# Kernel tuning notes

Hardware: AMD Instinct MI355X
Metric: run time of the kernel (lower is better)

Reference implementation:

```python
import jax, jax.numpy as jnp
import numpy as np

B, T, D = 4, 8160, 1024
N, H = 8, 128            # heads, units_per_head (D == N*H)
W = 12                   # block_size
LEFT_CTX = 13            # atten_left_context
L = LEFT_CTX - 1         # left context frames beyond current position
R = 0                    # atten_right_context
C = W + L + R            # context_size = 24
CAP = 50.0               # attention_logits_soft_capping


def _timing_signal(pos, channels):
    # sinusoidal embedding, channels even (1024)
    pos = pos.astype(jnp.float32)
    nt = channels // 2
    inc = np.log(10000.0) / max(nt - 1, 1)
    inv = jnp.exp(jnp.arange(nt, dtype=jnp.float32) * -inc)
    st = pos[:, :, None] * inv[None, None, :]
    return jnp.concatenate([jnp.sin(st), jnp.cos(st)], axis=2)


def _extract_block_context(x, block_size, left, right, pad_val):
    # x: [B, T, ...] -> [B, num_blocks, context_size, ...]
    pads = [(0, 0)] * x.ndim
    pads[1] = (left, right + block_size - 1)
    xp = jnp.pad(x, pads, constant_values=jnp.asarray(pad_val, x.dtype))
    frame_len = block_size + left + right
    num_frames = (xp.shape[1] - frame_len) // block_size + 1
    idx = jnp.arange(num_frames)[:, None] * block_size + jnp.arange(frame_len)[None, :]
    return jnp.take(xp, idx, axis=1)


def _convert_to_block(x, block_size):
    b, t = x.shape[0], x.shape[1]
    nb = t // block_size  # T chosen as multiple of block_size
    return x.reshape((b, nb, block_size) + x.shape[2:])


def setup_inputs() -> dict:
    key = jax.random.key(0)
    ks = jax.random.split(key, 6)
    x = jax.random.normal(ks[0], (B, T, D), dtype=jnp.float32)
    mask = jnp.ones((B, T), dtype=bool)
    i = jnp.arange(W)[:, None]
    j = jnp.arange(C)[None, :]
    causal_valid_mask = (j >= i) & (j - i <= L + R)  # [W, C]
    s = 1.0 / np.sqrt(D)
    wq = jax.random.normal(ks[1], (D, D), dtype=jnp.float32) * s
    wk = jax.random.normal(ks[2], (D, D), dtype=jnp.float32) * s
    wv = jax.random.normal(ks[3], (D, D), dtype=jnp.float32) * s
    pos_proj = jax.random.normal(ks[4], (D, N, H), dtype=jnp.float32) * s
    return {"x": x, "mask": mask, "causal_valid_mask": causal_valid_mask,
            "wq": wq, "wk": wk, "wv": wv, "pos_proj": pos_proj}


def reference(x, mask, causal_valid_mask, wq, wk, wv, pos_proj):
    b, t, d = x.shape
    u = t // W
    q = jnp.einsum('btd,df->btf', x, wq).reshape(b, t, N, H)
    k = jnp.einsum('btd,df->btf', x, wk).reshape(b, t, N, H)
    v = jnp.einsum('btd,df->btf', x, wv).reshape(b, t, N, H)

    q_blk = _convert_to_block(q, W) * (H ** -0.5)        # [B,U,W,N,H]
    k_ctx = _extract_block_context(k, W, L, R, 0.0)      # [B,U,C,N,H]
    v_ctx = _extract_block_context(v, W, L, R, 0.0)      # [B,U,C,N,H]

    # term A+C: content logits
    term_ac = jnp.einsum('BuwNH,BucNH->BNuwc', q_blk, k_ctx)

    # term B+D: relative position logits via skew trick
    pos = jnp.arange(L, -R - 1, -1)[None, :]             # [1, L+R+1]
    sin_emb = _timing_signal(pos, D)                     # [1, L+R+1, D]
    sin_emb = jnp.einsum('fd,dnh->fnh', sin_emb[0], pos_proj)  # [F,N,H]
    term_bd = jnp.einsum('BuwNH,FNH->BNuwF', q_blk, sin_emb)   # [B,N,U,W,F]
    term_bd = jnp.pad(term_bd, ((0, 0),) * 4 + ((0, C + 1 - (L + R + 1)),))
    term_bd = term_bd.reshape(b, N, u, W * (C + 1))[:, :, :, :W * C]
    term_bd = term_bd.reshape(b, N, u, W, C)

    logits = term_ac + term_bd
    logits = CAP * jnp.tanh(logits / CAP)

    mask_ctx = _extract_block_context(mask, W, L, R, False)    # [B,U,C]
    valid = mask_ctx[:, None, :, None, :] & causal_valid_mask[None, None, None, :, :]
    logits = jnp.where(valid, logits, jnp.asarray(-1e9, logits.dtype))
    probs = jax.nn.softmax(logits, axis=-1)              # [B,N,U,W,C]

    out = jnp.einsum('BNuwc,BucNH->BuwNH', probs, v_ctx)
    return out.reshape(b, u * W, N, H)[:, :t]            # [B,T,N,H]
```

## Files before the change

### kernel.cpp

```cpp
#include <hip/hip_runtime.h>
#include <cstdint>
#include <cstddef>


typedef __bf16 bf16_t;
typedef float  floatx4 __attribute__((ext_vector_type(4)));
typedef __bf16 bf16x8  __attribute__((ext_vector_type(8)));
typedef __bf16 bf16x4  __attribute__((ext_vector_type(4)));
typedef _Float16 f16x8 __attribute__((ext_vector_type(8)));

#define GLDS16(gp, lp)                                                        \
  __builtin_amdgcn_global_load_lds(                                           \
      (const __attribute__((address_space(1))) void*)(gp),                    \
      (__attribute__((address_space(3))) void*)(lp), 16, 0, 0)

static constexpr int kT     = 8160;
static constexpr int kM     = 4 * kT;
static constexpr int kU     = kT / 12;
static constexpr int kNC    = 3200;

__global__ __launch_bounds__(256) void convert_x(const float* __restrict__ X,
                                                 bf16_t* __restrict__ Xb) {
  const size_t i = ((size_t)blockIdx.x * 256 + threadIdx.x) * 8;
  float4 a = *(const float4*)(X + i);
  float4 b = *(const float4*)(X + i + 4);
  bf16x8 o;
  o[0] = (bf16_t)a.x; o[1] = (bf16_t)a.y; o[2] = (bf16_t)a.z; o[3] = (bf16_t)a.w;
  o[4] = (bf16_t)b.x; o[5] = (bf16_t)b.y; o[6] = (bf16_t)b.z; o[7] = (bf16_t)b.w;
  *(bf16x8*)(Xb + i) = o;
}

__global__ __launch_bounds__(512) void posemb_k(const float* __restrict__ pp,
                                                float* __restrict__ pe) {
  __shared__ float st[1024];
  __shared__ float red[4][128];
  const int d   = blockIdx.x;
  const int fc  = blockIdx.y;
  const int tid = threadIdx.x;
  const float dpos = (float)d;
  for (int i = tid; i < 1024; i += 512) {
    int idx = i & 511;
    float freq = expf(-(float)idx * (9.2103403719761836f / 511.0f));
    float a = dpos * freq;
    st[i] = (i < 512) ? sinf(a) : cosf(a);
  }
  __syncthreads();
  const int part = tid >> 7;
  const int fl   = tid & 127;
  const int f    = fc * 128 + fl;
  float acc = 0.f;
  const int dd0 = part * 256;
  for (int dd = dd0; dd < dd0 + 256; ++dd)
    acc += st[dd] * pp[(size_t)dd * 1024 + f];
  red[part][fl] = acc;
  __syncthreads();
  if (tid < 128)
    pe[(size_t)d * 1024 + f] = red[0][fl] + red[1][fl] + red[2][fl] + red[3][fl];
}

__global__ __launch_bounds__(256) void transpose_w(const float* __restrict__ Wq,
                                                   const float* __restrict__ Wk,
                                                   const float* __restrict__ Wv,
                                                   bf16_t* __restrict__ Wt) {
  __shared__ float tile[64][65];
  const int g = blockIdx.z;
  const float* W = (g == 0) ? Wq : (g == 1) ? Wk : Wv;
  bf16_t* O = Wt + (size_t)g * 1024 * 1024;
  const int k0 = blockIdx.x * 64, n0 = blockIdx.y * 64;
  const int col = threadIdx.x & 63, r4 = threadIdx.x >> 6;
#pragma unroll
  for (int i = 0; i < 16; ++i) {
    int row = i * 4 + r4;
    tile[row][col] = W[(size_t)(k0 + row) * 1024 + n0 + col];
  }
  __syncthreads();
#pragma unroll
  for (int i = 0; i < 16; ++i) {
    int row = i * 4 + r4;
    O[(size_t)(n0 + row) * 1024 + k0 + col] = (bf16_t)tile[col][row];
  }
}

__global__ __launch_bounds__(256) void pe2w(const float* __restrict__ pe,
                                            bf16_t* __restrict__ Wt) {
  const int idx = blockIdx.x;
  const int tid = threadIdx.x;
  bf16_t* out = Wt + (size_t)(3072 + idx) * 1024;
  if (idx >= 104) {
    bf16x4 z = {};
    *(bf16x4*)(out + tid * 4) = z;
    return;
  }
  const int n = idx / 13, d = idx - n * 13;
  __shared__ float peh[128];
  if (tid < 128) peh[tid] = pe[(size_t)d * 1024 + n * 128 + tid];
  __syncthreads();
  float acc[4] = {};
  const bf16_t* wb = Wt + (size_t)(n * 128) * 1024 + tid * 4;
  for (int h = 0; h < 128; ++h) {
    bf16x4 w4 = *(const bf16x4*)(wb + (size_t)h * 1024);
    float s = peh[h];
    acc[0] += s * (float)w4[0];
    acc[1] += s * (float)w4[1];
    acc[2] += s * (float)w4[2];
    acc[3] += s * (float)w4[3];
  }
  bf16x4 o;
  o[0] = (bf16_t)acc[0]; o[1] = (bf16_t)acc[1];
  o[2] = (bf16_t)acc[2]; o[3] = (bf16_t)acc[3];
  *(bf16x4*)(out + tid * 4) = o;
}

__global__ __launch_bounds__(512, 2) void qkv_gemm(const bf16_t* __restrict__ X,
                                                   const bf16_t* __restrict__ Wt,
                                                   bf16_t* __restrict__ QKV) {
  __shared__ __align__(16) bf16_t lds[8][8192];

  const int flat = blockIdx.x;
  const int work = (flat & 7) * 208 + (flat >> 3);
  const int mt = work / 13, nt = work % 13;
  const int m0 = mt * 256, n0 = nt * 256;

  const int tid  = threadIdx.x;
  const int wave = tid >> 6;
  const int lane = tid & 63;
  const int wm   = wave >> 2;
  const int wn   = wave & 3;
  const int qd   = lane >> 4;
  const int lr   = lane & 15;

  const int rr  = tid >> 3;
  const int cg8 = ((tid & 7) ^ (rr & 7)) * 8;
  const bf16_t* aP[4];
  const bf16_t* bP[4];
  {
    int r2 = m0 + 128 + rr, r3 = m0 + 192 + rr;
    aP[0] = X + (size_t)(m0 + rr) * 1024 + cg8;
    aP[1] = X + (size_t)(m0 + 64 + rr) * 1024 + cg8;
    aP[2] = X + (size_t)(r2 < kM ? r2 : 0) * 1024 + cg8;
    aP[3] = X + (size_t)(r3 < kM ? r3 : 0) * 1024 + cg8;
    int s2 = n0 + 128 + rr, s3 = n0 + 192 + rr;
    bP[0] = Wt + (size_t)(n0 + rr) * 1024 + cg8;
    bP[1] = Wt + (size_t)(n0 + 64 + rr) * 1024 + cg8;
    bP[2] = Wt + (size_t)(s2 < kNC ? s2 : 0) * 1024 + cg8;
    bP[3] = Wt + (size_t)(s3 < kNC ? s3 : 0) * 1024 + cg8;
  }

#define STAGE_A(h, t)                                                          \
  do {                                                                         \
    bf16_t* d_ = &lds[((t) & 1) * 4 + (h)][wave * 512];                        \
    GLDS16(aP[2 * (h)]     + (size_t)(t) * 64, d_);                            \
    GLDS16(aP[2 * (h) + 1] + (size_t)(t) * 64, d_ + 4096);                     \
  } while (0)
#define STAGE_B(h, t)                                                          \
  do {                                                                         \
    bf16_t* d_ = &lds[((t) & 1) * 4 + 2 + (h)][wave * 512];                    \
    GLDS16(bP[2 * (h)]     + (size_t)(t) * 64, d_);                            \
    GLDS16(bP[2 * (h) + 1] + (size_t)(t) * 64, d_ + 4096);                     \
  } while (0)

  auto frag = [&](int slot, int r, int cb) -> bf16x8 {
    uint32_t off = (uint32_t)(r * 128 + cb) ^ (uint32_t)((r & 7) << 4);
    return *(const bf16x8*)((const char*)&lds[slot][0] + off);
  };

  floatx4 acc[8][4] = {};

  STAGE_A(0, 0); STAGE_A(1, 0); STAGE_B(0, 0); STAGE_B(1, 0);
  STAGE_B(0, 1); STAGE_B(1, 1);
  asm volatile("s_waitcnt vmcnt(4)" ::: "memory");
  __builtin_amdgcn_s_barrier();

  const int aslot0 = wm;
  const int bslot0 = 2 + (wn >> 1);
  const int brow0  = (wn & 1) * 64;

#pragma unroll 2
  for (int t = 0; t < 16; ++t) {
    const int par = (t & 1) * 4;
    bf16x8 bfrag[4][2];
#pragma unroll
    for (int p = 0; p < 4; ++p) {
      if (p == 0) {
#pragma unroll
        for (int in = 0; in < 4; ++in)
#pragma unroll
          for (int k2 = 0; k2 < 2; ++k2)
            bfrag[in][k2] =
                frag(par + bslot0, brow0 + in * 16 + lr, k2 * 64 + qd * 16);
      }
      bf16x8 afrag[2][2];
#pragma unroll
      for (int i = 0; i < 2; ++i)
#pragma unroll
        for (int k2 = 0; k2 < 2; ++k2)
          afrag[i][k2] =
              frag(par + aslot0, (2 * p + i) * 16 + lr, k2 * 64 + qd * 16);

      if (p == 0)      { if (t < 15) STAGE_A(0, t + 1); }
      else if (p == 1) { if (t < 15) STAGE_A(1, t + 1); }
      else if (p == 2) { if (t < 14) STAGE_B(0, t + 2); }
      else             { if (t < 14) STAGE_B(1, t + 2); }

      if (p == 3) {
        if (t < 14) asm volatile("s_waitcnt vmcnt(4)" ::: "memory");
        else        asm volatile("s_waitcnt vmcnt(0)" ::: "memory");
      }
      __builtin_amdgcn_s_barrier();
      asm volatile("s_waitcnt lgkmcnt(0)" ::: "memory");
      __builtin_amdgcn_sched_barrier(0);

      __builtin_amdgcn_s_setprio(1);
#pragma unroll
      for (int i = 0; i < 2; ++i)
#pragma unroll
        for (int in = 0; in < 4; ++in)
#pragma unroll
          for (int k2 = 0; k2 < 2; ++k2)
            acc[2 * p + i][in] = __builtin_amdgcn_mfma_f32_16x16x32_bf16(
                afrag[i][k2], bfrag[in][k2], acc[2 * p + i][in], 0, 0, 0);
      __builtin_amdgcn_s_setprio(0);
      __builtin_amdgcn_sched_barrier(0);
      __builtin_amdgcn_s_barrier();
    }
  }
#undef STAGE_A
#undef STAGE_B

  const int mBase = m0 + wm * 128 + qd * 4;
  const int nBase = n0 + wn * 64 + lr;
  if (m0 + 256 <= kM && n0 + 256 <= kNC) {
#pragma unroll
    for (int im = 0; im < 8; ++im)
#pragma unroll
      for (int in = 0; in < 4; ++in)
#pragma unroll
        for (int r = 0; r < 4; ++r)
          QKV[(size_t)(mBase + im * 16 + r) * kNC + nBase + in * 16] =
              (bf16_t)acc[im][in][r];
  } else {
#pragma unroll
    for (int im = 0; im < 8; ++im)
#pragma unroll
      for (int in = 0; in < 4; ++in)
#pragma unroll
        for (int r = 0; r < 4; ++r) {
          int m = mBase + im * 16 + r;
          int n = nBase + in * 16;
          if (m < kM && n < kNC)
            QKV[(size_t)m * kNC + n] = (bf16_t)acc[im][in][r];
        }
  }
}

__global__ __launch_bounds__(256) void attn_k(const bf16_t* __restrict__ QKV,
                                              float* __restrict__ OUT) {
  __shared__ __align__(16) bf16_t  Ks[80 * 128];
  __shared__ __align__(16) _Float16 Vt[128 * 128];
  __shared__ __align__(16) unsigned char QP[64 * 256];
  __shared__ float qpes[64 * 16];

  bf16_t*   Qs = (bf16_t*)QP;
  _Float16* Ps = (_Float16*)QP;

  const int flat  = blockIdx.x;
  const int work  = (flat & 7) * 544 + (flat >> 3);
  const int strip = work >> 5;
  const int rest  = work & 31;
  const int n     = rest >> 2;
  const int b     = rest & 3;
  const int u0    = strip * 5;
  const int t0    = u0 * 12 - 12;
  const size_t bbase = (size_t)b * kT;
  const int tid  = threadIdx.x;
  const int mi   = tid >> 6;
  const int lane = tid & 63;
  const int qd   = lane >> 4;
  const int lr   = lane & 15;

  for (int i = tid; i < 64 * 16; i += 256) {
    int row = i >> 4, ch = i & 15;
    bf16x8 q8 = {};
    if (row < 60)
      q8 = *(const bf16x8*)(QKV + (bbase + (u0 * 12 + row)) * kNC + n * 128 + ch * 8);
    int idx = (row * 128 + ch * 8) ^ ((row & 7) << 3);
    *(bf16x8*)(Qs + idx) = q8;
  }
  for (int i = tid; i < 80 * 16; i += 256) {
    int row = i >> 4, ch = i & 15;
    int t = t0 + row;
    bf16x8 k8 = {};
    if (t >= 0 && t < kT)
      k8 = *(const bf16x8*)(QKV + (bbase + t) * kNC + 1024 + n * 128 + ch * 8);
    int idx = (row * 128 + ch * 8) ^ ((row & 7) << 3);
    *(bf16x8*)(Ks + idx) = k8;
  }
  for (int i = tid; i < 96 * 16; i += 256) {
    int c = i >> 4, ch = i & 15;
    int t = t0 + c;
    bf16x8 v8 = {};
    if (c < 80 && t >= 0 && t < kT)
      v8 = *(const bf16x8*)(QKV + (bbase + t) * kNC + 2048 + n * 128 + ch * 8);
#pragma unroll
    for (int jx = 0; jx < 8; ++jx) {
      int h = ch * 8 + jx;
      int idx = (h * 128 + c) ^ ((h & 7) << 3);
      Vt[idx] = (_Float16)(float)v8[jx];
    }
  }
  for (int i = tid; i < 780; i += 256) {
    int m = i / 13, d = i - m * 13;
    qpes[m * 16 + d] =
        (float)QKV[(bbase + (u0 * 12 + m)) * kNC + 3072 + n * 13 + d];
  }
  __syncthreads();

  floatx4 sAcc[2] = {};
  {
    bf16x8 aQ[4];
    const int qrow = mi * 16 + lr;
#pragma unroll
    for (int kk = 0; kk < 4; ++kk) {
      int idx = (qrow * 128 + kk * 32 + qd * 8) ^ ((qrow & 7) << 3);
      aQ[kk] = *(const bf16x8*)(Qs + idx);
    }
#pragma unroll
    for (int ci = 0; ci < 2; ++ci) {
      int krow = (mi + ci) * 16 + lr;
#pragma unroll
      for (int kk = 0; kk < 4; ++kk) {
        int idx = (krow * 128 + kk * 32 + qd * 8) ^ ((krow & 7) << 3);
        bf16x8 bK = *(const bf16x8*)(Ks + idx);
        sAcc[ci] = __builtin_amdgcn_mfma_f32_16x16x32_bf16(aQ[kk], bK, sAcc[ci], 0, 0, 0);
      }
    }
  }

  float pval[2][4];
#pragma unroll
  for (int r = 0; r < 4; ++r) {
    const int m = mi * 16 + qd * 4 + r;
    float sv[2]; bool val[2];
    float mx = -1e30f;
#pragma unroll
    for (int ci = 0; ci < 2; ++ci) {
      int c = (mi + ci) * 16 + lr;
      int d = m + 12 - c;
      int t = t0 + c;
      bool v = (d >= 0) && (d <= 12) && (t >= 0) && (m < 60);
      int qidx = m * 16 + (v ? d : 0);
      float s = (sAcc[ci][r] + qpes[qidx]) * 0.0017677669529663689f;
      s = 50.0f * tanhf(s);
      sv[ci] = v ? s : -1e30f;
      val[ci] = v;
      mx = fmaxf(mx, sv[ci]);
    }
    mx = fmaxf(mx, __shfl_xor(mx, 1));
    mx = fmaxf(mx, __shfl_xor(mx, 2));
    mx = fmaxf(mx, __shfl_xor(mx, 4));
    mx = fmaxf(mx, __shfl_xor(mx, 8));
    float e0 = val[0] ? __expf(sv[0] - mx) : 0.f;
    float e1 = val[1] ? __expf(sv[1] - mx) : 0.f;
    float sm = e0 + e1;
    sm += __shfl_xor(sm, 1);
    sm += __shfl_xor(sm, 2);
    sm += __shfl_xor(sm, 4);
    sm += __shfl_xor(sm, 8);
    float inv = (sm > 0.f) ? 1.0f / sm : 0.f;
    pval[0][r] = e0 * inv;
    pval[1][r] = e1 * inv;
  }

  __syncthreads();
  {
    float4 z = {};
    float4* p4 = (float4*)QP;
    for (int i = tid; i < 1024; i += 256) p4[i] = z;
  }
  __syncthreads();
#pragma unroll
  for (int r = 0; r < 4; ++r) {
    const int m = mi * 16 + qd * 4 + r;
#pragma unroll
    for (int ci = 0; ci < 2; ++ci) {
      int c = (mi + ci) * 16 + lr;
      int idx = (m * 128 + c) ^ ((m & 7) << 3);
      Ps[idx] = (_Float16)pval[ci][r];
    }
  }
  __syncthreads();

  floatx4 oAcc[8] = {};
  const int klo = mi >> 1;
  const int khi = (16 * mi + 27) >> 5;
  const int prow = mi * 16 + lr;
  for (int kk = klo; kk <= khi; ++kk) {
    int pidx = (prow * 128 + kk * 32 + qd * 8) ^ ((prow & 7) << 3);
    f16x8 aP = *(const f16x8*)(Ps + pidx);
#pragma unroll
    for (int hf = 0; hf < 8; ++hf) {
      int vrow = hf * 16 + lr;
      int vidx = (vrow * 128 + kk * 32 + qd * 8) ^ ((vrow & 7) << 3);
      f16x8 bV = *(const f16x8*)(Vt + vidx);
      oAcc[hf] = __builtin_amdgcn_mfma_f32_16x16x32_f16(aP, bV, oAcc[hf], 0, 0, 0);
    }
  }

#pragma unroll
  for (int r = 0; r < 4; ++r) {
    const int m = mi * 16 + qd * 4 + r;
    if (m < 60) {
      float* op = OUT + (bbase + (u0 * 12 + m)) * 1024 + n * 128 + lr;
#pragma unroll
      for (int hf = 0; hf < 8; ++hf)
        op[hf * 16] = oAcc[hf][r];
    }
  }
}

extern "C" void kernel_launch(void* const* d_in, const int* in_sizes, int n_in,
                              void* d_out, int out_size, void* d_ws, size_t ws_size,
                              hipStream_t stream) {
  const float* x  = (const float*)d_in[0];
  const float* wq = (const float*)d_in[3];
  const float* wk = (const float*)d_in[4];
  const float* wv = (const float*)d_in[5];
  const float* pp = (const float*)d_in[6];

  char* ws = (char*)d_ws;
  float*  pe  = (float*)ws;
  bf16_t* Wt  = (bf16_t*)(ws + (1u << 16));
  bf16_t* Xb  = (bf16_t*)(ws + (1u << 16) + 8u * 1024 * 1024);
  bf16_t* QKV = (bf16_t*)(ws + (1u << 16) + 8u * 1024 * 1024 +
                          (size_t)kM * 1024 * 2);
  float* out = (float*)d_out;

  convert_x<<<kM * 1024 / (256 * 8), 256, 0, stream>>>(x, Xb);
  posemb_k<<<dim3(13, 8), 512, 0, stream>>>(pp, pe);
  transpose_w<<<dim3(16, 16, 3), 256, 0, stream>>>(wq, wk, wv, Wt);
  pe2w<<<128, 256, 0, stream>>>(pe, Wt);
  qkv_gemm<<<1664, 512, 0, stream>>>(Xb, Wt, QKV);
  attn_k<<<4352, 256, 0, stream>>>(QKV, out);
}
```

Baseline: 650.8 us.

## Split attention into QK-softmax and banded PV kernels with compact probabilities

Splits the fused attention kernel into two kernels. The first computes QK logits and softmax and writes only the 13 valid banded probabilities per query to a global buffer that reuses the bf16 X workspace. The second computes the PV product as a 13-tap banded sum in fp32 on the vector ALUs. This removes the large transposed-V LDS staging and the mostly-zero PV MFMA. Q loads now go straight to registers, and tanh is computed with exp and no max subtraction. The cost is an extra launch, a global round trip for the probabilities, and softmax with no max shift (safe only because the logits are capped at 50).

After: 588.5 us. -9.6%, faster.

```diff
diff --git a/kernel.cpp b/kernel.cpp
--- a/kernel.cpp
+++ b/kernel.cpp
@@ -7,7 +7,6 @@
 typedef float  floatx4 __attribute__((ext_vector_type(4)));
 typedef __bf16 bf16x8  __attribute__((ext_vector_type(8)));
 typedef __bf16 bf16x4  __attribute__((ext_vector_type(4)));
-typedef _Float16 f16x8 __attribute__((ext_vector_type(8)));
 
 #define GLDS16(gp, lp)                                                        \
   __builtin_amdgcn_global_load_lds(                                           \
@@ -253,15 +252,10 @@
   }
 }
 
-__global__ __launch_bounds__(256) void attn_k(const bf16_t* __restrict__ QKV,
-                                              float* __restrict__ OUT) {
-  __shared__ __align__(16) bf16_t  Ks[80 * 128];
-  __shared__ __align__(16) _Float16 Vt[128 * 128];
-  __shared__ __align__(16) unsigned char QP[64 * 256];
+__global__ __launch_bounds__(256) void qk_soft(const bf16_t* __restrict__ QKV,
+                                               float* __restrict__ Pg) {
+  __shared__ __align__(16) bf16_t Ks[80 * 128];
   __shared__ float qpes[64 * 16];
-
-  bf16_t*   Qs = (bf16_t*)QP;
-  _Float16* Ps = (_Float16*)QP;
 
   const int flat  = blockIdx.x;
   const int work  = (flat & 7) * 544 + (flat >> 3);
@@ -272,41 +266,31 @@
   const int u0    = strip * 5;
   const int t0    = u0 * 12 - 12;
   const size_t bbase = (size_t)b * kT;
+  const int bn    = b * 8 + n;
   const int tid  = threadIdx.x;
   const int mi   = tid >> 6;
   const int lane = tid & 63;
   const int qd   = lane >> 4;
   const int lr   = lane & 15;
 
-  for (int i = tid; i < 64 * 16; i += 256) {
-    int row = i >> 4, ch = i & 15;
-    bf16x8 q8 = {};
-    if (row < 60)
-      q8 = *(const bf16x8*)(QKV + (bbase + (u0 * 12 + row)) * kNC + n * 128 + ch * 8);
-    int idx = (row * 128 + ch * 8) ^ ((row & 7) << 3);
-    *(bf16x8*)(Qs + idx) = q8;
-  }
+  bf16x8 aQ[4];
+  {
+    int tq = u0 * 12 + mi * 16 + lr;
+    if (tq > kT - 1) tq = kT - 1;
+    const bf16_t* qg = QKV + (bbase + tq) * kNC + n * 128;
+#pragma unroll
+    for (int kk = 0; kk < 4; ++kk)
+      aQ[kk] = *(const bf16x8*)(qg + kk * 32 + qd * 8);
+  }
+
   for (int i = tid; i < 80 * 16; i += 256) {
     int row = i >> 4, ch = i & 15;
-    int t = t0 + row;
+    int kt = t0 + row;
     bf16x8 k8 = {};
-    if (t >= 0 && t < kT)
-      k8 = *(const bf16x8*)(QKV + (bbase + t) * kNC + 1024 + n * 128 + ch * 8);
+    if (kt >= 0 && kt < kT)
+      k8 = *(const bf16x8*)(QKV + (bbase + kt) * kNC + 1024 + n * 128 + ch * 8);
     int idx = (row * 128 + ch * 8) ^ ((row & 7) << 3);
     *(bf16x8*)(Ks + idx) = k8;
-  }
-  for (int i = tid; i < 96 * 16; i += 256) {
-    int c = i >> 4, ch = i & 15;
-    int t = t0 + c;
-    bf16x8 v8 = {};
-    if (c < 80 && t >= 0 && t < kT)
-      v8 = *(const bf16x8*)(QKV + (bbase + t) * kNC + 2048 + n * 128 + ch * 8);
-#pragma unroll
-    for (int jx = 0; jx < 8; ++jx) {
-      int h = ch * 8 + jx;
-      int idx = (h * 128 + c) ^ ((h & 7) << 3);
-      Vt[idx] = (_Float16)(float)v8[jx];
-    }
   }
   for (int i = tid; i < 780; i += 256) {
     int m = i / 13, d = i - m * 13;
@@ -316,105 +300,96 @@
   __syncthreads();
 
   floatx4 sAcc[2] = {};
-  {
-    bf16x8 aQ[4];
-    const int qrow = mi * 16 + lr;
+#pragma unroll
+  for (int ci = 0; ci < 2; ++ci) {
+    int krow = (mi + ci) * 16 + lr;
 #pragma unroll
     for (int kk = 0; kk < 4; ++kk) {
-      int idx = (qrow * 128 + kk * 32 + qd * 8) ^ ((qrow & 7) << 3);
-      aQ[kk] = *(const bf16x8*)(Qs + idx);
-    }
-#pragma unroll
-    for (int ci = 0; ci < 2; ++ci) {
-      int krow = (mi + ci) * 16 + lr;
-#pragma unroll
-      for (int kk = 0; kk < 4; ++kk) {
-        int idx = (krow * 128 + kk * 32 + qd * 8) ^ ((krow & 7) << 3);
-        bf16x8 bK = *(const bf16x8*)(Ks + idx);
-        sAcc[ci] = __builtin_amdgcn_mfma_f32_16x16x32_bf16(aQ[kk], bK, sAcc[ci], 0, 0, 0);
-      }
-    }
-  }
-
-  float pval[2][4];
+      int idx = (krow * 128 + kk * 32 + qd * 8) ^ ((krow & 7) << 3);
+      bf16x8 bK = *(const bf16x8*)(Ks + idx);
+      sAcc[ci] = __builtin_amdgcn_mfma_f32_16x16x32_bf16(aQ[kk], bK, sAcc[ci], 0, 0, 0);
+    }
+  }
+
 #pragma unroll
   for (int r = 0; r < 4; ++r) {
     const int m = mi * 16 + qd * 4 + r;
-    float sv[2]; bool val[2];
-    float mx = -1e30f;
+    float e[2];
 #pragma unroll
     for (int ci = 0; ci < 2; ++ci) {
       int c = (mi + ci) * 16 + lr;
       int d = m + 12 - c;
-      int t = t0 + c;
-      bool v = (d >= 0) && (d <= 12) && (t >= 0) && (m < 60);
+      int kt = t0 + c;
+      bool v = (d >= 0) && (d <= 12) && (kt >= 0) && (m < 60);
       int qidx = m * 16 + (v ? d : 0);
       float s = (sAcc[ci][r] + qpes[qidx]) * 0.0017677669529663689f;
-      s = 50.0f * tanhf(s);
-      sv[ci] = v ? s : -1e30f;
-      val[ci] = v;
-      mx = fmaxf(mx, sv[ci]);
-    }
-    mx = fmaxf(mx, __shfl_xor(mx, 1));
-    mx = fmaxf(mx, __shfl_xor(mx, 2));
-    mx = fmaxf(mx, __shfl_xor(mx, 4));
-    mx = fmaxf(mx, __shfl_xor(mx, 8));
-    float e0 = val[0] ? __expf(sv[0] - mx) : 0.f;
-    float e1 = val[1] ? __expf(sv[1] - mx) : 0.f;
-    float sm = e0 + e1;
+      float t2 = __expf(2.0f * s);
+      float th = 1.0f - 2.0f / (t2 + 1.0f);
+      e[ci] = v ? __expf(50.0f * th) : 0.0f;
+    }
+    float sm = e[0] + e[1];
     sm += __shfl_xor(sm, 1);
     sm += __shfl_xor(sm, 2);
     sm += __shfl_xor(sm, 4);
     sm += __shfl_xor(sm, 8);
-    float inv = (sm > 0.f) ? 1.0f / sm : 0.f;
-    pval[0][r] = e0 * inv;
-    pval[1][r] = e1 * inv;
-  }
-
-  __syncthreads();
-  {
-    float4 z = {};
-    float4* p4 = (float4*)QP;
-    for (int i = tid; i < 1024; i += 256) p4[i] = z;
-  }
-  __syncthreads();
-#pragma unroll
-  for (int r = 0; r < 4; ++r) {
-    const int m = mi * 16 + qd * 4 + r;
+    float iv = 1.0f / sm;
 #pragma unroll
     for (int ci = 0; ci < 2; ++ci) {
       int c = (mi + ci) * 16 + lr;
-      int idx = (m * 128 + c) ^ ((m & 7) << 3);
-      Ps[idx] = (_Float16)pval[ci][r];
-    }
-  }
-  __syncthreads();
-
-  floatx4 oAcc[8] = {};
-  const int klo = mi >> 1;
-  const int khi = (16 * mi + 27) >> 5;
-  const int prow = mi * 16 + lr;
-  for (int kk = klo; kk <= khi; ++kk) {
-    int pidx = (prow * 128 + kk * 32 + qd * 8) ^ ((prow & 7) << 3);
-    f16x8 aP = *(const f16x8*)(Ps + pidx);
-#pragma unroll
-    for (int hf = 0; hf < 8; ++hf) {
-      int vrow = hf * 16 + lr;
-      int vidx = (vrow * 128 + kk * 32 + qd * 8) ^ ((vrow & 7) << 3);
-      f16x8 bV = *(const f16x8*)(Vt + vidx);
-      oAcc[hf] = __builtin_amdgcn_mfma_f32_16x16x32_f16(aP, bV, oAcc[hf], 0, 0, 0);
-    }
-  }
-
-#pragma unroll
-  for (int r = 0; r < 4; ++r) {
-    const int m = mi * 16 + qd * 4 + r;
-    if (m < 60) {
-      float* op = OUT + (bbase + (u0 * 12 + m)) * 1024 + n * 128 + lr;
-#pragma unroll
-      for (int hf = 0; hf < 8; ++hf)
-        op[hf * 16] = oAcc[hf][r];
-    }
+      int d = m + 12 - c;
+      if (m < 60 && d >= 0 && d <= 12)
+        Pg[((size_t)bn * kT + (u0 * 12 + m)) * 16 + d] = e[ci] * iv;
+    }
+  }
+}
+
+__global__ __launch_bounds__(256) void pv_k(const bf16_t* __restrict__ QKV,
+                                            const float* __restrict__ Pg,
+                                            float* __restrict__ OUT) {
+  __shared__ float Vs[60 * 132];
+  __shared__ float ps[48 * 16];
+
+  const int flat = blockIdx.x;
+  const int work = (flat & 7) * 680 + (flat >> 3);
+  const int bn = work / 170, ts = work % 170;
+  const int b  = bn >> 3, n = bn & 7;
+  const int t1 = ts * 48;
+  const size_t bbase = (size_t)b * kT;
+  const int tid = threadIdx.x;
+
+  for (int i = tid; i < 60 * 16; i += 256) {
+    int r = i >> 4, ch = i & 15;
+    int kt = t1 - 12 + r;
+    int vo = r * 132 + ch * 8;
+    if (kt < 0) {
+      float4 z = {};
+      *(float4*)(Vs + vo) = z; *(float4*)(Vs + vo + 4) = z;
+    } else {
+      bf16x8 v8 = *(const bf16x8*)(QKV + (bbase + kt) * kNC + 2048 + n * 128 + ch * 8);
+      float4 vl = { (float)v8[0], (float)v8[1], (float)v8[2], (float)v8[3] };
+      float4 vh = { (float)v8[4], (float)v8[5], (float)v8[6], (float)v8[7] };
+      *(float4*)(Vs + vo) = vl; *(float4*)(Vs + vo + 4) = vh;
+    }
+  }
+  if (tid < 192) {
+    int r = tid >> 2, q4 = tid & 3;
+    float4 p4 = *(const float4*)(Pg + ((size_t)bn * kT + t1 + r) * 16 + q4 * 4);
+    *(float4*)(ps + r * 16 + q4 * 4) = p4;
+  }
+  __syncthreads();
+
+  for (int i = tid; i < 48 * 32; i += 256) {
+    int lt = i >> 5, c4 = i & 31;
+    const float* pw = ps + lt * 16;
+    float4 acc = {};
+#pragma unroll
+    for (int d = 0; d <= 12; ++d) {
+      float pd = pw[d];
+      float4 v4 = *(const float4*)(Vs + (lt + 12 - d) * 132 + c4 * 4);
+      acc.x += pd * v4.x; acc.y += pd * v4.y;
+      acc.z += pd * v4.z; acc.w += pd * v4.w;
+    }
+    *(float4*)(OUT + (bbase + t1 + lt) * 1024 + n * 128 + c4 * 4) = acc;
   }
 }
 
@@ -433,6 +408,7 @@
   bf16_t* Xb  = (bf16_t*)(ws + (1u << 16) + 8u * 1024 * 1024);
   bf16_t* QKV = (bf16_t*)(ws + (1u << 16) + 8u * 1024 * 1024 +
                           (size_t)kM * 1024 * 2);
+  float* Pg = (float*)Xb;
   float* out = (float*)d_out;
 
   convert_x<<<kM * 1024 / (256 * 8), 256, 0, stream>>>(x, Xb);
@@ -440,5 +416,6 @@
   transpose_w<<<dim3(16, 16, 3), 256, 0, stream>>>(wq, wk, wv, Wt);
   pe2w<<<128, 256, 0, stream>>>(pe, Wt);
   qkv_gemm<<<1664, 512, 0, stream>>>(Xb, Wt, QKV);
-  attn_k<<<4352, 256, 0, stream>>>(QKV, out);
-}
+  qk_soft<<<4352, 256, 0, stream>>>(QKV, Pg);
+  pv_k<<<5440, 256, 0, stream>>>(QKV, Pg, out);
+}
```
